# Optimization experiments

Measured on AMD Instinct MI355X. Metric: run time of the kernel, lower is better.

## Reference

```python
import jax, jax.numpy as jnp
import numpy as np

B, HW, C = 32, 56, 128
WS, SS, NH = 7, 3, 4
HD = C // NH
SCALE = HD ** -0.5
NWIN = (HW // WS) ** 2  # 64 windows per image
N = WS * WS             # 49 tokens per window


def _build_constants():
    # relative position index [N, N] into flattened (13*13) bias table
    coords = np.stack(np.meshgrid(np.arange(WS), np.arange(WS), indexing='ij'))  # [2,7,7]
    cf = coords.reshape(2, -1)                       # [2,49]
    rel = cf[:, :, None] - cf[:, None, :]            # [2,49,49]
    rel = rel.transpose(1, 2, 0).copy()              # [49,49,2]
    rel[:, :, 0] += WS - 1
    rel[:, :, 1] += WS - 1
    rel[:, :, 0] *= 2 * WS - 1
    pos_index = rel.sum(-1)                          # [49,49]
    # shifted-window attention mask [nW, N, N]
    img = np.zeros((HW, HW))
    sl = (slice(0, -WS), slice(-WS, -SS), slice(-SS, None))
    cnt = 0
    for h in sl:
        for w in sl:
            img[h, w] = cnt
            cnt += 1
    mw = img.reshape(HW // WS, WS, HW // WS, WS).transpose(0, 2, 1, 3).reshape(NWIN, N)
    am = mw[:, None, :] - mw[:, :, None]             # unsqueeze(1) - unsqueeze(2)
    am = np.where(am != 0, -100.0, 0.0).astype(np.float32)
    return jnp.asarray(pos_index), jnp.asarray(am)

POS_INDEX, ATTN_MASK = _build_constants()


def _ln(x, w, b, eps=1e-5):
    mu = x.mean(-1, keepdims=True)
    var = ((x - mu) ** 2).mean(-1, keepdims=True)
    return (x - mu) * jax.lax.rsqrt(var + eps) * w + b


def setup_inputs() -> dict:
    key = jax.random.key(0)
    ks = jax.random.split(key, 10)
    s = 0.02
    return {
        'x': jax.random.normal(ks[0], (B, HW * HW, C), jnp.float32),
        'norm1_w': jnp.ones((C,), jnp.float32),
        'norm1_b': jnp.zeros((C,), jnp.float32),
        'qkv_w': jax.random.normal(ks[1], (C, 3 * C), jnp.float32) * s,
        'qkv_b': jax.random.normal(ks[2], (3 * C,), jnp.float32) * s,
        'proj_w': jax.random.normal(ks[3], (C, C), jnp.float32) * s,
        'proj_b': jax.random.normal(ks[4], (C,), jnp.float32) * s,
        'pos_bias_table': jax.random.normal(ks[5], (2 * WS - 1, 2 * WS - 1, NH), jnp.float32) * s,
        'mlp_w1': jax.random.normal(ks[6], (C, 4 * C), jnp.float32) * s,
        'mlp_b1': jnp.zeros((4 * C,), jnp.float32),
        'mlp_w2': jax.random.normal(ks[7], (4 * C, C), jnp.float32) * s,
        'mlp_b2': jnp.zeros((C,), jnp.float32),
        'norm2_w': jnp.ones((C,), jnp.float32),
        'norm2_b': jnp.zeros((C,), jnp.float32),
    }


def reference(x, norm1_w, norm1_b, qkv_w, qkv_b, proj_w, proj_b, pos_bias_table,
              mlp_w1, mlp_b1, mlp_w2, mlp_b2, norm2_w, norm2_b):
    G = HW // WS  # grid of windows per side
    Bw = B * NWIN
    shortcut = x
    y = _ln(x, norm1_w, norm1_b).reshape(B, HW, HW, C)
    # cyclic shift
    y = jnp.roll(y, (-SS, -SS), axis=(1, 2))
    # window partition -> [B*nW, 49, C]
    yw = y.reshape(B, G, WS, G, WS, C).transpose(0, 1, 3, 2, 4, 5).reshape(Bw, N, C)
    # qkv projection
    qkv = (yw @ qkv_w + qkv_b).reshape(Bw, N, 3, NH, HD).transpose(2, 0, 3, 1, 4)
    q, k, v = qkv[0] * SCALE, qkv[1], qkv[2]  # [Bw, NH, N, HD]
    attn = jnp.einsum('bhnd,bhmd->bhnm', q, k)
    # relative position bias [NH, N, N]
    bias = pos_bias_table.reshape(-1, NH)[POS_INDEX]  # [N,N,NH]
    attn = attn + bias.transpose(2, 0, 1)[None]
    # shift mask per window
    attn = attn.reshape(B, NWIN, NH, N, N) + ATTN_MASK[None, :, None]
    attn = jax.nn.softmax(attn.reshape(Bw, NH, N, N), axis=-1)
    out = jnp.einsum('bhnm,bhmd->bhnd', attn, v).transpose(0, 2, 1, 3).reshape(Bw, N, C)
    out = out @ proj_w + proj_b
    # window reverse
    out = out.reshape(B, G, G, WS, WS, C).transpose(0, 1, 3, 2, 4, 5).reshape(B, HW, HW, C)
    out = jnp.roll(out, (SS, SS), axis=(1, 2)).reshape(B, HW * HW, C)
    x = shortcut + out
    h = _ln(x, norm2_w, norm2_b)
    h = jax.nn.gelu(h @ mlp_w1 + mlp_b1, approximate=False) @ mlp_w2 + mlp_b2
    return x + h
```

## Files before the change

### kernel.cpp

```cpp
#include <hip/hip_runtime.h>
#include <hip/hip_bf16.h>

#define NTOK 100352
#define SCALE_Q 0.17677669529663687f

typedef __bf16 bf16x8 __attribute__((ext_vector_type(8)));
typedef float f32x4 __attribute__((ext_vector_type(4)));
struct bf2 { __hip_bfloat16 x, y; };

__device__ __forceinline__ int wt_to_tok(int wt) {
  int w = wt / 49, n = wt - w * 49;
  int b = w >> 6, wi = w & 63;
  int gh = wi >> 3, gw = wi & 7;
  int r = n / 7, c = n - r * 7;
  int hs = gh * 7 + r + 3; if (hs >= 56) hs -= 56;
  int ws = gw * 7 + c + 3; if (ws >= 56) ws -= 56;
  return (b * 56 + hs) * 56 + ws;
}

__device__ __forceinline__ float gelu_sig(float v) {
  return v / (1.0f + __expf(-1.702f * v));
}

__global__ __launch_bounds__(256) void prep_all(const float* __restrict__ qkvw,
                                                const float* __restrict__ projw,
                                                const float* __restrict__ w1,
                                                const float* __restrict__ w2,
                                                __hip_bfloat16* __restrict__ dst) {
  int i = blockIdx.x * 256 + threadIdx.x;
  float v;
  if (i < 49152) { int n = i >> 7, k = i & 127; v = qkvw[k * 384 + n]; }
  else if (i < 65536) { int j = i - 49152; int n = j >> 7, k = j & 127; v = projw[k * 128 + n]; }
  else if (i < 131072) { int j = i - 65536; int n = j >> 7, k = j & 127; v = w1[k * 512 + n]; }
  else { int j = i - 131072; int n = j / 512, k = j - n * 512; v = w2[k * 128 + n]; }
  dst[i] = __float2bfloat16(v);
}

__global__ __launch_bounds__(256) void ln1_apply(const float* __restrict__ x,
                                                 const float* __restrict__ nw,
                                                 const float* __restrict__ nb,
                                                 __hip_bfloat16* __restrict__ xn) {
  int wt = blockIdx.x * 4 + (threadIdx.x >> 6);
  int lane = threadIdx.x & 63;
  int tok = wt_to_tok(wt);
  float2 v = *(const float2*)(x + (size_t)tok * 128 + lane * 2);
  float s = v.x + v.y, ss = v.x * v.x + v.y * v.y;
#pragma unroll
  for (int off = 32; off; off >>= 1) {
    s += __shfl_xor(s, off);
    ss += __shfl_xor(ss, off);
  }
  float mu = s * (1.0f / 128.0f);
  float rstd = rsqrtf(ss * (1.0f / 128.0f) - mu * mu + 1e-5f);
  float2 wv = *(const float2*)(nw + lane * 2);
  float2 bv = *(const float2*)(nb + lane * 2);
  bf2 o;
  o.x = __float2bfloat16((v.x - mu) * rstd * wv.x + bv.x);
  o.y = __float2bfloat16((v.y - mu) * rstd * wv.y + bv.y);
  *(bf2*)(xn + (size_t)wt * 128 + lane * 2) = o;
}

__global__ __launch_bounds__(256) void attn_mfma(const __hip_bfloat16* __restrict__ qkv,
                                                 const float* __restrict__ ptab,
                                                 __hip_bfloat16* __restrict__ attnout) {
  __shared__ __align__(16) char lds[4 * 12288];
  const int tid = threadIdx.x;
  const int lane = tid & 63, h = tid >> 6;
  const int w = blockIdx.x;
  const int wi = w & 63, gh = wi >> 3, gw = wi & 7;
  char* Pl = lds + h * 12288;
  char* VTl = Pl + 8192;
  const int lxi = lane & 15, lq = lane >> 4, lg4 = (lane >> 4) * 4;

  const __hip_bfloat16* base = qkv + (size_t)w * 49 * 384 + h * 32;
  __hip_bfloat16* op = attnout + (size_t)w * 49 * 128 + h * 32;

  bf16x8 qa[4], kb[4];
#pragma unroll
  for (int mi = 0; mi < 4; ++mi) {
    int t = mi * 16 + lxi; if (t > 48) t = 48;
    qa[mi] = *(const bf16x8*)(base + (size_t)t * 384 + lq * 8);
    kb[mi] = *(const bf16x8*)(base + (size_t)t * 384 + 128 + lq * 8);
  }
  {
    union { bf16x8 v; __hip_bfloat16 e[8]; } vv[4];
    const __hip_bfloat16* vp = base + (size_t)(lane < 49 ? lane : 0) * 384 + 256;
#pragma unroll
    for (int q = 0; q < 4; ++q) vv[q].v = *(const bf16x8*)(vp + q * 8);
    __hip_bfloat16 z = __float2bfloat16(0.0f);
#pragma unroll
    for (int q = 0; q < 4; ++q)
#pragma unroll
      for (int e = 0; e < 8; ++e) {
        int d = q * 8 + e;
        __hip_bfloat16 val = (lane < 49) ? vv[q].e[e] : z;
        *(__hip_bfloat16*)(VTl + d * 128 + ((lane * 2) ^ ((d & 7) << 4))) = val;
      }
  }

  f32x4 s[4][4] = {};
#pragma unroll
  for (int mi = 0; mi < 4; ++mi)
#pragma unroll
    for (int ni = 0; ni < 4; ++ni)
      s[mi][ni] = __builtin_amdgcn_mfma_f32_16x16x32_bf16(qa[mi], kb[ni], s[mi][ni], 0, 0, 0);

  int rj[4], cj[4], cntj[4], jbad[4];
#pragma unroll
  for (int ni = 0; ni < 4; ++ni) {
    int jc = ni * 16 + lxi;
    jbad[ni] = (jc > 48);
    int jj = jbad[ni] ? 48 : jc;
    rj[ni] = jj / 7; cj[ni] = jj - rj[ni] * 7;
    int hj = gh * 7 + rj[ni], wj = gw * 7 + cj[ni];
    cntj[ni] = (hj < 49 ? 0 : (hj < 53 ? 3 : 6)) + (wj < 49 ? 0 : (wj < 53 ? 1 : 2));
  }
#pragma unroll
  for (int mi = 0; mi < 4; ++mi)
#pragma unroll
    for (int j = 0; j < 4; ++j) {
      int i = mi * 16 + lg4 + j; if (i > 48) i = 48;
      int ri = i / 7, ci = i - ri * 7;
      int hi_ = gh * 7 + ri, wi_ = gw * 7 + ci;
      int cnti = (hi_ < 49 ? 0 : (hi_ < 53 ? 3 : 6)) + (wi_ < 49 ? 0 : (wi_ < 53 ? 1 : 2));
#pragma unroll
      for (int ni = 0; ni < 4; ++ni) {
        float b = ptab[((ri - rj[ni] + 6) * 13 + (ci - cj[ni] + 6)) * 4 + h];
        float val = s[mi][ni][j] * SCALE_Q + b;
        if (cnti != cntj[ni]) val -= 100.0f;
        if (jbad[ni]) val = -1e30f;
        s[mi][ni][j] = val;
      }
    }

#pragma unroll
  for (int mi = 0; mi < 4; ++mi)
#pragma unroll
    for (int j = 0; j < 4; ++j) {
      float m = fmaxf(fmaxf(s[mi][0][j], s[mi][1][j]), fmaxf(s[mi][2][j], s[mi][3][j]));
#pragma unroll
      for (int off = 8; off; off >>= 1) m = fmaxf(m, __shfl_xor(m, off));
      float e[4], sum = 0.0f;
#pragma unroll
      for (int ni = 0; ni < 4; ++ni) { e[ni] = __expf(s[mi][ni][j] - m); sum += e[ni]; }
#pragma unroll
      for (int off = 8; off; off >>= 1) sum += __shfl_xor(sum, off);
      float inv = 1.0f / sum;
#pragma unroll
      for (int ni = 0; ni < 4; ++ni) s[mi][ni][j] = e[ni] * inv;
    }

#pragma unroll
  for (int mi = 0; mi < 4; ++mi)
#pragma unroll
    for (int j = 0; j < 4; ++j) {
      int row = mi * 16 + lg4 + j;
      int sw = (row & 7) << 4;
      char* prow = Pl + row * 128;
#pragma unroll
      for (int ni = 0; ni < 4; ++ni)
        *(__hip_bfloat16*)(prow + (((ni * 16 + lxi) * 2) ^ sw)) =
            __float2bfloat16(s[mi][ni][j]);
    }

  __syncthreads();

  f32x4 o[4][2] = {};
#pragma unroll
  for (int ks = 0; ks < 2; ++ks) {
    bf16x8 pa[4], vb[2];
#pragma unroll
    for (int mi = 0; mi < 4; ++mi) {
      int row = mi * 16 + lxi;
      pa[mi] = *(const bf16x8*)(Pl + row * 128 + ((ks * 64 + lq * 16) ^ ((row & 7) << 4)));
    }
#pragma unroll
    for (int ni = 0; ni < 2; ++ni) {
      int row = ni * 16 + lxi;
      vb[ni] = *(const bf16x8*)(VTl + row * 128 + ((ks * 64 + lq * 16) ^ ((row & 7) << 4)));
    }
#pragma unroll
    for (int mi = 0; mi < 4; ++mi)
#pragma unroll
      for (int ni = 0; ni < 2; ++ni)
        o[mi][ni] = __builtin_amdgcn_mfma_f32_16x16x32_bf16(pa[mi], vb[ni], o[mi][ni], 0, 0, 0);
  }

#pragma unroll
  for (int mi = 0; mi < 4; ++mi)
#pragma unroll
    for (int j = 0; j < 4; ++j) {
      int q = mi * 16 + lg4 + j;
      if (q < 49) {
#pragma unroll
        for (int ni = 0; ni < 2; ++ni)
          op[(size_t)q * 128 + ni * 16 + lxi] = __float2bfloat16(o[mi][ni][j]);
      }
    }
}

template<int EPI>
__global__ __launch_bounds__(256) void gemm_mfma(
    const __hip_bfloat16* __restrict__ A, int lda, int NB,
    const __hip_bfloat16* __restrict__ Wt,
    const float* __restrict__ bias,
    void* __restrict__ outv, int ldo,
    __hip_bfloat16* __restrict__ out2,
    const float* __restrict__ nw, const float* __restrict__ nb,
    const float* __restrict__ resf, const __hip_bfloat16* __restrict__ resb,
    int K)
{
  __shared__ __align__(16) char AsB[128 * 256];
  __shared__ float redS[256], redQ[256];
  const int bid = blockIdx.x;
  const int xcd = bid & 7, tt = bid >> 3;
  const int nbk = tt % NB, mseq = tt / NB;
  const int m0 = (mseq * 8 + xcd) * 128, n0 = nbk * 128;
  const int tid = threadIdx.x;
  const int srow = tid >> 1;
  const int scol = (tid & 1) * 64;
  const int lane = tid & 63, wid = tid >> 6;
  const int wm = wid >> 1, wn = wid & 1;
  const int lrow = lane & 15, lq = lane >> 4;

  f32x4 acc[4][4] = {};

  for (int k0 = 0; k0 < K; k0 += 128) {
    {
      const char* ap = (const char*)A + ((size_t)(m0 + srow) * lda + k0 + scol) * 2;
      char* dst = AsB + srow * 256;
      int sw = (srow & 7) << 4;
#pragma unroll
      for (int t = 0; t < 8; ++t) {
        int4 raw = *(const int4*)(ap + t * 16);
        *(int4*)(dst + ((scol * 2 + t * 16) ^ sw)) = raw;
      }
    }
    __syncthreads();
#pragma unroll
    for (int ks = 0; ks < 4; ++ks) {
      int kb = ks * 64 + lq * 16;
      bf16x8 af[4], bfr[4];
#pragma unroll
      for (int mi = 0; mi < 4; ++mi) {
        int r = wm * 64 + mi * 16 + lrow;
        af[mi] = *(const bf16x8*)(AsB + r * 256 + (kb ^ ((r & 7) << 4)));
      }
#pragma unroll
      for (int ni = 0; ni < 4; ++ni) {
        int n = n0 + wn * 64 + ni * 16 + lrow;
        bfr[ni] = *(const bf16x8*)(Wt + (size_t)n * K + k0 + ks * 32 + lq * 8);
      }
#pragma unroll
      for (int mi = 0; mi < 4; ++mi)
#pragma unroll
        for (int ni = 0; ni < 4; ++ni)
          acc[mi][ni] = __builtin_amdgcn_mfma_f32_16x16x32_bf16(af[mi], bfr[ni], acc[mi][ni], 0, 0, 0);
    }
    __syncthreads();
  }

  float bv[4];
#pragma unroll
  for (int ni = 0; ni < 4; ++ni) bv[ni] = bias[n0 + wn * 64 + ni * 16 + lrow];

  if (EPI == 4) {
    __hip_bfloat16* x2 = (__hip_bfloat16*)outv;
    float nwc[4], nbc[4];
#pragma unroll
    for (int ni = 0; ni < 4; ++ni) {
      int colg = wn * 64 + ni * 16 + lrow;
      nwc[ni] = nw[colg]; nbc[ni] = nb[colg];
    }
    int toks[4][4];
#pragma unroll
    for (int mi = 0; mi < 4; ++mi)
#pragma unroll
      for (int j = 0; j < 4; ++j) {
        int row = wm * 64 + mi * 16 + lq * 4 + j;
        int tok = wt_to_tok(m0 + row);
        toks[mi][j] = tok;
        float s = 0.0f, ss = 0.0f;
#pragma unroll
        for (int ni = 0; ni < 4; ++ni) {
          int colg = wn * 64 + ni * 16 + lrow;
          float val = acc[mi][ni][j] + bv[ni] + resf[(size_t)tok * 128 + colg];
          x2[(size_t)tok * 128 + colg] = __float2bfloat16(val);
          acc[mi][ni][j] = val;
          s += val; ss += val * val;
        }
#pragma unroll
        for (int off = 8; off; off >>= 1) {
          s += __shfl_xor(s, off);
          ss += __shfl_xor(ss, off);
        }
        if (lrow == 0) { redS[row * 2 + wn] = s; redQ[row * 2 + wn] = ss; }
      }
    __syncthreads();
#pragma unroll
    for (int mi = 0; mi < 4; ++mi)
#pragma unroll
      for (int j = 0; j < 4; ++j) {
        int row = wm * 64 + mi * 16 + lq * 4 + j;
        float s = redS[row * 2] + redS[row * 2 + 1];
        float ss = redQ[row * 2] + redQ[row * 2 + 1];
        float mu = s * (1.0f / 128.0f);
        float rstd = rsqrtf(ss * (1.0f / 128.0f) - mu * mu + 1e-5f);
        int tok = toks[mi][j];
#pragma unroll
        for (int ni = 0; ni < 4; ++ni) {
          int colg = wn * 64 + ni * 16 + lrow;
          float xnv = (acc[mi][ni][j] - mu) * rstd * nwc[ni] + nbc[ni];
          out2[(size_t)tok * 128 + colg] = __float2bfloat16(xnv);
        }
      }
    return;
  }

#pragma unroll
  for (int mi = 0; mi < 4; ++mi) {
#pragma unroll
    for (int j = 0; j < 4; ++j) {
      int rowg = m0 + wm * 64 + mi * 16 + lq * 4 + j;
#pragma unroll
      for (int ni = 0; ni < 4; ++ni) {
        int colg = n0 + wn * 64 + ni * 16 + lrow;
        float val = acc[mi][ni][j] + bv[ni];
        if (EPI == 0) {
          ((__hip_bfloat16*)outv)[(size_t)rowg * ldo + colg] = __float2bfloat16(val);
        } else if (EPI == 1) {
          ((__hip_bfloat16*)outv)[(size_t)rowg * ldo + colg] = __float2bfloat16(gelu_sig(val));
        } else {
          float r = __bfloat162float(resb[(size_t)rowg * 128 + colg]);
          ((float*)outv)[(size_t)rowg * 128 + colg] = val + r;
        }
      }
    }
  }
}

extern "C" void kernel_launch(void* const* d_in, const int* in_sizes, int n_in,
                              void* d_out, int out_size, void* d_ws, size_t ws_size,
                              hipStream_t stream) {
  (void)in_sizes; (void)n_in; (void)out_size; (void)ws_size;
  const float* x     = (const float*)d_in[0];
  const float* n1w   = (const float*)d_in[1];
  const float* n1b   = (const float*)d_in[2];
  const float* qkvw  = (const float*)d_in[3];
  const float* qkvb  = (const float*)d_in[4];
  const float* projw = (const float*)d_in[5];
  const float* projb = (const float*)d_in[6];
  const float* ptab  = (const float*)d_in[7];
  const float* w1    = (const float*)d_in[8];
  const float* b1    = (const float*)d_in[9];
  const float* w2    = (const float*)d_in[10];
  const float* b2    = (const float*)d_in[11];
  const float* n2w   = (const float*)d_in[12];
  const float* n2b   = (const float*)d_in[13];
  float* out = (float*)d_out;

  char* ws = (char*)d_ws;
  __hip_bfloat16* xn      = (__hip_bfloat16*)ws;
  __hip_bfloat16* qkv     = (__hip_bfloat16*)(ws + 25690112);
  __hip_bfloat16* attnout = (__hip_bfloat16*)(ws + 102760448);
  __hip_bfloat16* u       = (__hip_bfloat16*)(ws + 25690112);
  __hip_bfloat16* x2      = (__hip_bfloat16*)(ws + 128450560);
  __hip_bfloat16* x2n     = (__hip_bfloat16*)(ws + 154140672);
  __hip_bfloat16* wbase   = (__hip_bfloat16*)(ws + 179830784);
  __hip_bfloat16* qkvwT  = wbase;
  __hip_bfloat16* projwT = wbase + 49152;
  __hip_bfloat16* w1T    = wbase + 65536;
  __hip_bfloat16* w2T    = wbase + 131072;

  prep_all<<<768, 256, 0, stream>>>(qkvw, projw, w1, w2, wbase);
  ln1_apply<<<NTOK / 4, 256, 0, stream>>>(x, n1w, n1b, xn);
  gemm_mfma<0><<<2352, 256, 0, stream>>>(xn, 128, 3, qkvwT, qkvb,
                                         qkv, 384, nullptr, nullptr, nullptr,
                                         nullptr, nullptr, 128);
  attn_mfma<<<2048, 256, 0, stream>>>(qkv, ptab, attnout);
  gemm_mfma<4><<<784, 256, 0, stream>>>(attnout, 128, 1, projwT, projb,
                                        x2, 128, x2n, n2w, n2b, x, nullptr, 128);
  gemm_mfma<1><<<3136, 256, 0, stream>>>(x2n, 128, 4, w1T, b1,
                                         (void*)u, 512, nullptr, nullptr, nullptr,
                                         nullptr, nullptr, 128);
  gemm_mfma<3><<<784, 256, 0, stream>>>(u, 512, 1, w2T, b2,
                                        out, 128, nullptr, nullptr, nullptr,
                                        nullptr, x2, 512);
}
```

Measured before the change: 268.8 us.

## Loop over N chunks per block to reuse staged A tile in GEMMs

GEMMs whose N spans several 128-column tiles (QKV and MLP up-projection) now launch one block per 128-row M tile. Each block stages A into shared memory once and loops over all N chunks, instead of launching a separate block per (M,N) pair that reloads A each time. K and chunk count become template parameters, and the XCD-aware block remapping is removed. This cuts redundant A loads and block count, at the cost of fewer, longer blocks (784), less parallelism, and the loss of the XCD-local L2 mapping.

```diff
diff --git a/kernel.cpp b/kernel.cpp
--- a/kernel.cpp
+++ b/kernel.cpp
@@ -199,23 +199,19 @@
     }
 }
 
-template<int EPI>
-__global__ __launch_bounds__(256) void gemm_mfma(
-    const __hip_bfloat16* __restrict__ A, int lda, int NB,
+template<int NCHUNK, int K, int EPI>
+__global__ __launch_bounds__(256) void gemm_nloop(
+    const __hip_bfloat16* __restrict__ A, int lda,
     const __hip_bfloat16* __restrict__ Wt,
     const float* __restrict__ bias,
     void* __restrict__ outv, int ldo,
     __hip_bfloat16* __restrict__ out2,
     const float* __restrict__ nw, const float* __restrict__ nb,
-    const float* __restrict__ resf, const __hip_bfloat16* __restrict__ resb,
-    int K)
+    const float* __restrict__ resf, const __hip_bfloat16* __restrict__ resb)
 {
   __shared__ __align__(16) char AsB[128 * 256];
   __shared__ float redS[256], redQ[256];
-  const int bid = blockIdx.x;
-  const int xcd = bid & 7, tt = bid >> 3;
-  const int nbk = tt % NB, mseq = tt / NB;
-  const int m0 = (mseq * 8 + xcd) * 128, n0 = nbk * 128;
+  const int m0 = blockIdx.x * 128;
   const int tid = threadIdx.x;
   const int srow = tid >> 1;
   const int scol = (tid & 1) * 64;
@@ -223,8 +219,64 @@
   const int wm = wid >> 1, wn = wid & 1;
   const int lrow = lane & 15, lq = lane >> 4;
 
+  if (NCHUNK > 1) {
+    {
+      const char* ap = (const char*)A + ((size_t)(m0 + srow) * lda + scol) * 2;
+      char* dst = AsB + srow * 256;
+      int sw = (srow & 7) << 4;
+#pragma unroll
+      for (int t = 0; t < 8; ++t) {
+        int4 raw = *(const int4*)(ap + t * 16);
+        *(int4*)(dst + ((scol * 2 + t * 16) ^ sw)) = raw;
+      }
+    }
+    __syncthreads();
+
+    for (int nc = 0; nc < NCHUNK; ++nc) {
+      const int n0 = nc * 128;
+      f32x4 acc[4][4] = {};
+#pragma unroll
+      for (int ks = 0; ks < 4; ++ks) {
+        int kb = ks * 64 + lq * 16;
+        bf16x8 af[4], bfr[4];
+#pragma unroll
+        for (int mi = 0; mi < 4; ++mi) {
+          int r = wm * 64 + mi * 16 + lrow;
+          af[mi] = *(const bf16x8*)(AsB + r * 256 + (kb ^ ((r & 7) << 4)));
+        }
+#pragma unroll
+        for (int ni = 0; ni < 4; ++ni) {
+          int n = n0 + wn * 64 + ni * 16 + lrow;
+          bfr[ni] = *(const bf16x8*)(Wt + (size_t)n * 128 + ks * 32 + lq * 8);
+        }
+#pragma unroll
+        for (int mi = 0; mi < 4; ++mi)
+#pragma unroll
+          for (int ni = 0; ni < 4; ++ni)
+            acc[mi][ni] = __builtin_amdgcn_mfma_f32_16x16x32_bf16(af[mi], bfr[ni], acc[mi][ni], 0, 0, 0);
+      }
+      float bv[4];
+#pragma unroll
+      for (int ni = 0; ni < 4; ++ni) bv[ni] = bias[n0 + wn * 64 + ni * 16 + lrow];
+#pragma unroll
+      for (int mi = 0; mi < 4; ++mi) {
+#pragma unroll
+        for (int j = 0; j < 4; ++j) {
+          int rowg = m0 + wm * 64 + mi * 16 + lq * 4 + j;
+#pragma unroll
+          for (int ni = 0; ni < 4; ++ni) {
+            int colg = n0 + wn * 64 + ni * 16 + lrow;
+            float val = acc[mi][ni][j] + bv[ni];
+            if (EPI == 1) val = gelu_sig(val);
+            ((__hip_bfloat16*)outv)[(size_t)rowg * ldo + colg] = __float2bfloat16(val);
+          }
+        }
+      }
+    }
+    return;
+  }
+
   f32x4 acc[4][4] = {};
-
   for (int k0 = 0; k0 < K; k0 += 128) {
     {
       const char* ap = (const char*)A + ((size_t)(m0 + srow) * lda + k0 + scol) * 2;
@@ -248,7 +300,7 @@
       }
 #pragma unroll
       for (int ni = 0; ni < 4; ++ni) {
-        int n = n0 + wn * 64 + ni * 16 + lrow;
+        int n = wn * 64 + ni * 16 + lrow;
         bfr[ni] = *(const bf16x8*)(Wt + (size_t)n * K + k0 + ks * 32 + lq * 8);
       }
 #pragma unroll
@@ -262,7 +314,7 @@
 
   float bv[4];
 #pragma unroll
-  for (int ni = 0; ni < 4; ++ni) bv[ni] = bias[n0 + wn * 64 + ni * 16 + lrow];
+  for (int ni = 0; ni < 4; ++ni) bv[ni] = bias[wn * 64 + ni * 16 + lrow];
 
   if (EPI == 4) {
     __hip_bfloat16* x2 = (__hip_bfloat16*)outv;
@@ -324,16 +376,10 @@
       int rowg = m0 + wm * 64 + mi * 16 + lq * 4 + j;
 #pragma unroll
       for (int ni = 0; ni < 4; ++ni) {
-        int colg = n0 + wn * 64 + ni * 16 + lrow;
+        int colg = wn * 64 + ni * 16 + lrow;
         float val = acc[mi][ni][j] + bv[ni];
-        if (EPI == 0) {
-          ((__hip_bfloat16*)outv)[(size_t)rowg * ldo + colg] = __float2bfloat16(val);
-        } else if (EPI == 1) {
-          ((__hip_bfloat16*)outv)[(size_t)rowg * ldo + colg] = __float2bfloat16(gelu_sig(val));
-        } else {
-          float r = __bfloat162float(resb[(size_t)rowg * 128 + colg]);
-          ((float*)outv)[(size_t)rowg * 128 + colg] = val + r;
-        }
+        float r = __bfloat162float(resb[(size_t)rowg * 128 + colg]);
+        ((float*)outv)[(size_t)rowg * 128 + colg] = val + r;
       }
     }
   }
@@ -374,16 +420,16 @@
 
   prep_all<<<768, 256, 0, stream>>>(qkvw, projw, w1, w2, wbase);
   ln1_apply<<<NTOK / 4, 256, 0, stream>>>(x, n1w, n1b, xn);
-  gemm_mfma<0><<<2352, 256, 0, stream>>>(xn, 128, 3, qkvwT, qkvb,
-                                         qkv, 384, nullptr, nullptr, nullptr,
-                                         nullptr, nullptr, 128);
+  gemm_nloop<3, 128, 0><<<784, 256, 0, stream>>>(xn, 128, qkvwT, qkvb,
+                                                 qkv, 384, nullptr, nullptr, nullptr,
+                                                 nullptr, nullptr);
   attn_mfma<<<2048, 256, 0, stream>>>(qkv, ptab, attnout);
-  gemm_mfma<4><<<784, 256, 0, stream>>>(attnout, 128, 1, projwT, projb,
-                                        x2, 128, x2n, n2w, n2b, x, nullptr, 128);
-  gemm_mfma<1><<<3136, 256, 0, stream>>>(x2n, 128, 4, w1T, b1,
-                                         (void*)u, 512, nullptr, nullptr, nullptr,
-                                         nullptr, nullptr, 128);
-  gemm_mfma<3><<<784, 256, 0, stream>>>(u, 512, 1, w2T, b2,
-                                        out, 128, nullptr, nullptr, nullptr,
-                                        nullptr, x2, 512);
-}
+  gemm_nloop<1, 128, 4><<<784, 256, 0, stream>>>(attnout, 128, projwT, projb,
+                                                 x2, 128, x2n, n2w, n2b, x, nullptr);
+  gemm_nloop<4, 128, 1><<<784, 256, 0, stream>>>(x2n, 128, w1T, b1,
+                                                 (void*)u, 512, nullptr, nullptr, nullptr,
+                                                 nullptr, nullptr);
+  gemm_nloop<1, 512, 3><<<784, 256, 0, stream>>>(u, 512, w2T, b2,
+                                                 out, 128, nullptr, nullptr, nullptr,
+                                                 nullptr, x2);
+}
```

New measurement: 308.2 us. +14.7%, slower.
